# Kernel tuning notes

Hardware: AMD Instinct MI355X
Metric: run time of the kernel (lower is better)

## Reference

```python
import jax, jax.numpy as jnp
import numpy as np

B, SQ, SKV, D = 8, 2048, 2048, 1024

def setup_inputs() -> dict:
    key = jax.random.key(0)
    ks = jax.random.split(key, 8)
    s = 1.0 / np.sqrt(D)  # torch Linear default init range
    return {
        "target": jax.random.normal(ks[0], (B, SQ, D), dtype=jnp.float32),
        "non_target": jax.random.normal(ks[1], (B, SKV, D), dtype=jnp.float32),
        "Wq": jax.random.uniform(ks[2], (D, D), jnp.float32, -s, s),
        "bq": jax.random.uniform(ks[3], (D,), jnp.float32, -s, s),
        "Wk": jax.random.uniform(ks[4], (D, D), jnp.float32, -s, s),
        "bk": jax.random.uniform(ks[5], (D,), jnp.float32, -s, s),
        "Wv": jax.random.uniform(ks[6], (D, D), jnp.float32, -s, s),
        "bv": jax.random.uniform(ks[7], (D,), jnp.float32, -s, s),
    }

def reference(target, non_target, Wq, bq, Wk, bk, Wv, bv):
    # Linear projections (torch Linear: x @ W.T + b)
    q = jnp.einsum('bsd,ed->bse', target, Wq) + bq       # [B,SQ,D]
    k = jnp.einsum('bsd,ed->bse', non_target, Wk) + bk   # [B,SKV,D]
    v = jnp.einsum('bsd,ed->bse', non_target, Wv) + bv   # [B,SKV,D]
    # Unscaled attention, exactly as the original module (no 1/sqrt(d))
    scores = jnp.einsum('bqd,bkd->bqk', q, k)            # [B,SQ,SKV]
    weights = jax.nn.softmax(scores, axis=-1)
    return jnp.einsum('bqk,bkd->bqd', weights, v)        # [B,SQ,D]
```

## Files before the change

### kernel.cpp

```cpp
#include <hip/hip_runtime.h>


typedef _Float16 half8 __attribute__((ext_vector_type(8)));
typedef _Float16 half4v __attribute__((ext_vector_type(4)));
typedef float floatx4 __attribute__((ext_vector_type(4)));

__device__ __forceinline__ void async_copy16(const _Float16* g, _Float16* l) {
  __builtin_amdgcn_global_load_lds(
      (const __attribute__((address_space(1))) void*)g,
      (__attribute__((address_space(3))) void*)l,
      16, 0, 0);
}

__global__ __launch_bounds__(256) void cast_f32_f16(const float* __restrict__ src,
                                                    _Float16* __restrict__ dst, long n) {
  long i = ((long)blockIdx.x * 256 + threadIdx.x) * 8;
  if (i >= n) return;
  float4 a = *(const float4*)(src + i);
  float4 b = *(const float4*)(src + i + 4);
  half8 h;
  h[0] = (_Float16)a.x; h[1] = (_Float16)a.y; h[2] = (_Float16)a.z; h[3] = (_Float16)a.w;
  h[4] = (_Float16)b.x; h[5] = (_Float16)b.y; h[6] = (_Float16)b.z; h[7] = (_Float16)b.w;
  *(half8*)(dst + i) = h;
}


#define GSLICE(KC, AFC, BFC, AFN, BFN)                                          \
  {                                                                             \
    const int kc_ = (KC);                                                       \
    int ks_ = kc_ + 3; if (ks_ > NK - 1) ks_ = NK - 1;                          \
    int pf_ = kc_ + 1; if (pf_ > NK - 1) pf_ = NK - 1;                          \
    _Float16* sa_ = Ar + (ks_ & 3) * 8192 + ldst;                               \
    _Float16* sb_ = Br + (ks_ & 3) * 8192 + ldst;                               \
    const long go_ = (long)ks_ * 32;                                            \
    async_copy16(Abg + go_, sa_);                                               \
    async_copy16(Abg + go_ + lK128, sa_ + 4096);                                \
    async_copy16(Bbg + go_, sb_);                                               \
    async_copy16(Bbg + go_ + lK128, sb_ + 4096);                                \
    const _Float16* pa_ = Ar + (pf_ & 3) * 8192 + wm * 4096 + aoff;             \
    const _Float16* pb_ = Br + (pf_ & 3) * 8192 + wn * 2048 + aoff;             \
    _Pragma("unroll") for (int n = 0; n < 4; ++n)                               \
      BFN[n] = *(const half8*)(pb_ + n * 512);                                  \
    _Pragma("unroll") for (int i = 0; i < 8; ++i)                               \
      AFN[i] = *(const half8*)(pa_ + (i & 3) * 512 + (i >> 2) * 2048);          \
    __builtin_amdgcn_sched_barrier(0);                                          \
    __builtin_amdgcn_s_setprio(1);                                              \
    _Pragma("unroll") for (int i = 0; i < 8; ++i)                               \
      _Pragma("unroll") for (int n = 0; n < 4; ++n)                             \
        acc[i][n] = __builtin_amdgcn_mfma_f32_16x16x32_f16(AFC[i], BFC[n],      \
                                                           acc[i][n], 0, 0, 0); \
    __builtin_amdgcn_s_setprio(0);                                              \
    asm volatile("s_waitcnt lgkmcnt(0)" ::: "memory");                          \
    __builtin_amdgcn_sched_barrier(0);                                          \
    asm volatile("s_waitcnt vmcnt(4)" ::: "memory");                            \
    __builtin_amdgcn_s_barrier();                                               \
  }

template <int OMODE>
__global__ __launch_bounds__(512, 2) void gemm256(const _Float16* __restrict__ A,
                                                  const _Float16* __restrict__ Bm,
                                                  const float* __restrict__ bias,
                                                  void* __restrict__ out,
                                                  int K, int N,
                                                  long sA, long sB, long sO) {
  __shared__ __attribute__((aligned(16))) _Float16 lds[65536];
  _Float16* Ar = lds;
  _Float16* Br = lds + 32768;

  const int tid = threadIdx.x;
  const int lane = tid & 63;
  const int wave = tid >> 6;
  const int wm = wave >> 2;
  const int wn = wave & 3;
  const int frow = lane & 15;
  const int fq = (lane >> 4) & 3;
  const long bz = blockIdx.z;

  const int glog = (tid & 7) ^ ((tid >> 3) & 7);
  const long sg = (long)(2 * (tid >> 3) + (glog >> 2)) * K + (glog & 3) * 8;
  const int ldst = tid * 8;
  const long lK128 = (long)K * 128;

  const _Float16* Abg = A + bz * sA + (long)blockIdx.x * 256 * K + sg;
  const _Float16* Bbg = Bm + bz * sB + (long)blockIdx.y * 256 * K + sg;

  const int gphys = ((frow & 1) * 4 + fq) ^ (frow >> 1);
  const int aoff = (frow >> 1) * 64 + gphys * 8;

  floatx4 acc[8][4];
#pragma unroll
  for (int m = 0; m < 8; ++m)
#pragma unroll
    for (int n = 0; n < 4; ++n) acc[m][n] = (floatx4){0.f, 0.f, 0.f, 0.f};

  const int NK = K >> 5;

#pragma unroll
  for (int kp = 0; kp < 3; ++kp) {
    async_copy16(Abg + kp * 32, Ar + kp * 8192 + ldst);
    async_copy16(Abg + kp * 32 + lK128, Ar + kp * 8192 + ldst + 4096);
    async_copy16(Bbg + kp * 32, Br + kp * 8192 + ldst);
    async_copy16(Bbg + kp * 32 + lK128, Br + kp * 8192 + ldst + 4096);
  }
  asm volatile("s_waitcnt vmcnt(4)" ::: "memory");
  __builtin_amdgcn_s_barrier();

  half8 afA[8], bfA[4], afB[8], bfB[4];
  {
    const _Float16* pa = Ar + wm * 4096 + aoff;
    const _Float16* pb = Br + wn * 2048 + aoff;
#pragma unroll
    for (int n = 0; n < 4; ++n) bfA[n] = *(const half8*)(pb + n * 512);
#pragma unroll
    for (int i = 0; i < 8; ++i) afA[i] = *(const half8*)(pa + (i & 3) * 512 + (i >> 2) * 2048);
  }
  asm volatile("s_waitcnt lgkmcnt(0)" ::: "memory");
  __builtin_amdgcn_sched_barrier(0);

  for (int kc = 0; kc < NK; kc += 2) {
    GSLICE(kc, afA, bfA, afB, bfB);
    GSLICE(kc + 1, afB, bfB, afA, bfA);
  }

  if (OMODE == 0 || OMODE == 1) {
#pragma unroll
    for (int n = 0; n < 4; ++n) {
      const int cg = blockIdx.y * 256 + wn * 64 + n * 16 + frow;
      const float bvv = bias[cg];
#pragma unroll
      for (int m = 0; m < 8; ++m) {
        const int rg = blockIdx.x * 256 + wm * 128 + m * 16 + fq * 4;
        if (OMODE == 0) {
#pragma unroll
          for (int i = 0; i < 4; ++i)
            ((_Float16*)out)[(long)(rg + i) * N + cg] = (_Float16)(acc[m][n][i] + bvv);
        } else {
          const long bb = rg >> 11;
          const int s = rg & 2047;
          half4v hv;
#pragma unroll
          for (int i = 0; i < 4; ++i) hv[i] = (_Float16)(acc[m][n][i] + bvv);
          *(half4v*)((_Float16*)out + bb * (2048l * 1024) + (long)cg * 2048 + s) = hv;
        }
      }
    }
  } else {
#pragma unroll
    for (int n = 0; n < 4; ++n) {
      const int cg = blockIdx.y * 256 + wn * 64 + n * 16 + frow;
#pragma unroll
      for (int m = 0; m < 8; ++m) {
        const int rgl = blockIdx.x * 256 + wm * 128 + m * 16 + fq * 4;
#pragma unroll
        for (int i = 0; i < 4; ++i) {
          if (OMODE == 2)
            ((float*)out + bz * sO)[(long)(rgl + i) * N + cg] = acc[m][n][i];
          else
            ((_Float16*)out + bz * sO)[(long)(rgl + i) * N + cg] = (_Float16)acc[m][n][i];
        }
      }
    }
  }
}

__global__ __launch_bounds__(256) void softmax_rows(const _Float16* __restrict__ S,
                                                    _Float16* __restrict__ P) {
  const long row = blockIdx.x;
  const _Float16* src = S + row * 2048;
  _Float16* dst = P + row * 2048;
  const int tid = threadIdx.x;

  half8 v = ((const half8*)src)[tid];
  float f[8];
#pragma unroll
  for (int i = 0; i < 8; i++) f[i] = (float)v[i];

  float m = fmaxf(fmaxf(fmaxf(f[0], f[1]), fmaxf(f[2], f[3])),
                  fmaxf(fmaxf(f[4], f[5]), fmaxf(f[6], f[7])));
#pragma unroll
  for (int o = 32; o > 0; o >>= 1) m = fmaxf(m, __shfl_xor(m, o, 64));
  __shared__ float redm[4];
  if ((tid & 63) == 0) redm[tid >> 6] = m;
  __syncthreads();
  m = fmaxf(fmaxf(redm[0], redm[1]), fmaxf(redm[2], redm[3]));

  float e[8], s = 0.f;
#pragma unroll
  for (int i = 0; i < 8; i++) { e[i] = __expf(f[i] - m); s += e[i]; }
#pragma unroll
  for (int o = 32; o > 0; o >>= 1) s += __shfl_xor(s, o, 64);
  __shared__ float reds[4];
  if ((tid & 63) == 0) reds[tid >> 6] = s;
  __syncthreads();
  s = (reds[0] + reds[1]) + (reds[2] + reds[3]);
  const float inv = 1.f / s;

  half8 h;
#pragma unroll
  for (int i = 0; i < 8; i++) h[i] = (_Float16)(e[i] * inv);
  ((half8*)dst)[tid] = h;
}

extern "C" void kernel_launch(void* const* d_in, const int* in_sizes, int n_in,
                              void* d_out, int out_size, void* d_ws, size_t ws_size,
                              hipStream_t stream) {
  const float* target = (const float*)d_in[0];
  const float* non_target = (const float*)d_in[1];
  const float* Wq = (const float*)d_in[2];
  const float* bq = (const float*)d_in[3];
  const float* Wk = (const float*)d_in[4];
  const float* bk = (const float*)d_in[5];
  const float* Wv = (const float*)d_in[6];
  const float* bv = (const float*)d_in[7];

  char* ws = (char*)d_ws;
  const size_t MB = 1ull << 20;
  _Float16* tgt16 = (_Float16*)(ws);
  _Float16* ntg16 = (_Float16*)(ws + 32 * MB);
  _Float16* S16 = (_Float16*)(ws);
  _Float16* P16 = (_Float16*)(ws + 64 * MB);
  _Float16* Q16 = (_Float16*)(ws + 128 * MB);
  _Float16* K16 = (_Float16*)(ws + 160 * MB);
  _Float16* Vt16 = (_Float16*)(ws + 192 * MB);
  _Float16* Wq16 = (_Float16*)(ws + 224 * MB);
  _Float16* Wk16 = (_Float16*)(ws + 226 * MB);
  _Float16* Wv16 = (_Float16*)(ws + 228 * MB);

  const long nBig = 8l * 2048 * 1024;
  const long nW = 1024l * 1024;

  cast_f32_f16<<<8192, 256, 0, stream>>>(target, tgt16, nBig);
  cast_f32_f16<<<8192, 256, 0, stream>>>(non_target, ntg16, nBig);
  cast_f32_f16<<<512, 256, 0, stream>>>(Wq, Wq16, nW);
  cast_f32_f16<<<512, 256, 0, stream>>>(Wk, Wk16, nW);
  cast_f32_f16<<<512, 256, 0, stream>>>(Wv, Wv16, nW);

  gemm256<0><<<dim3(64, 4, 1), 512, 0, stream>>>(tgt16, Wq16, bq, Q16, 1024, 1024, 0, 0, 0);
  gemm256<0><<<dim3(64, 4, 1), 512, 0, stream>>>(ntg16, Wk16, bk, K16, 1024, 1024, 0, 0, 0);
  gemm256<1><<<dim3(64, 4, 1), 512, 0, stream>>>(ntg16, Wv16, bv, Vt16, 1024, 1024, 0, 0, 0);

  gemm256<3><<<dim3(8, 8, 8), 512, 0, stream>>>(Q16, K16, nullptr, S16, 1024, 2048,
                                                2048l * 1024, 2048l * 1024, 2048l * 2048);

  softmax_rows<<<16384, 256, 0, stream>>>(S16, P16);

  gemm256<2><<<dim3(8, 4, 8), 512, 0, stream>>>(P16, Vt16, nullptr, (float*)d_out, 2048, 1024,
                                                2048l * 2048, 1024l * 2048, 2048l * 1024);
}
```

Baseline: 488.3 us.

## Fuse input casts and softmax normalization into GEMM A-tile loads

The fp32-to-fp16 casts of target and non_target move into the projection GEMMs: the A tile is loaded as fp32 into registers, converted, and written to LDS instead of using async global-to-LDS copies. The softmax kernel now writes only per-row max and inverse sum, and the P·V GEMM applies exp and scaling while staging S into LDS, so the P buffer is never written or read. Block index swizzling is added to the score and output GEMMs to improve L2 reuse. The cost is register-path loads and extra ALU work inside the GEMM main loop, which may weaken the async pipeline's overlap. The exp is also recomputed once per column block of the output GEMM.

```diff
diff --git a/kernel.cpp b/kernel.cpp
--- a/kernel.cpp
+++ b/kernel.cpp
@@ -33,10 +33,21 @@
     _Float16* sa_ = Ar + (ks_ & 3) * 8192 + ldst;                               \
     _Float16* sb_ = Br + (ks_ & 3) * 8192 + ldst;                               \
     const long go_ = (long)ks_ * 32;                                            \
-    async_copy16(Abg + go_, sa_);                                               \
-    async_copy16(Abg + go_ + lK128, sa_ + 4096);                                \
-    async_copy16(Bbg + go_, sb_);                                               \
-    async_copy16(Bbg + go_ + lK128, sb_ + 4096);                                \
+    floatx4 qa0_, qa1_, qb0_, qb1_; half8 ha_, hb_;                             \
+    if (ATRANS == 0) {                                                          \
+      async_copy16(Ah + go_, sa_);                                              \
+      async_copy16(Ah + go_ + lK128, sa_ + 4096);                               \
+    } else if (ATRANS == 1) {                                                   \
+      qa0_ = *(const floatx4*)(Af + go_);                                       \
+      qa1_ = *(const floatx4*)(Af + go_ + 4);                                   \
+      qb0_ = *(const floatx4*)(Af + go_ + lK128);                               \
+      qb1_ = *(const floatx4*)(Af + go_ + lK128 + 4);                           \
+    } else {                                                                    \
+      ha_ = *(const half8*)(Ah + go_);                                          \
+      hb_ = *(const half8*)(Ah + go_ + lK128);                                  \
+    }                                                                           \
+    async_copy16(Bh + go_, sb_);                                                \
+    async_copy16(Bh + go_ + lK128, sb_ + 4096);                                 \
     const _Float16* pa_ = Ar + (pf_ & 3) * 8192 + wm * 4096 + aoff;             \
     const _Float16* pb_ = Br + (pf_ & 3) * 8192 + wn * 2048 + aoff;             \
     _Pragma("unroll") for (int n = 0; n < 4; ++n)                               \
@@ -50,16 +61,33 @@
         acc[i][n] = __builtin_amdgcn_mfma_f32_16x16x32_f16(AFC[i], BFC[n],      \
                                                            acc[i][n], 0, 0, 0); \
     __builtin_amdgcn_s_setprio(0);                                              \
+    __builtin_amdgcn_sched_barrier(0);                                          \
+    if (ATRANS == 1) {                                                          \
+      half8 w0_, w1_;                                                           \
+      _Pragma("unroll") for (int t = 0; t < 4; ++t) {                           \
+        w0_[t] = (_Float16)qa0_[t]; w0_[4 + t] = (_Float16)qa1_[t];             \
+        w1_[t] = (_Float16)qb0_[t]; w1_[4 + t] = (_Float16)qb1_[t]; }           \
+      *(half8*)sa_ = w0_; *(half8*)(sa_ + 4096) = w1_;                          \
+    } else if (ATRANS == 2) {                                                   \
+      half8 w0_, w1_;                                                           \
+      _Pragma("unroll") for (int t = 0; t < 8; ++t) {                           \
+        w0_[t] = (_Float16)(__expf((float)ha_[t] - mA0) * sA0);                 \
+        w1_[t] = (_Float16)(__expf((float)hb_[t] - mA1) * sA1); }               \
+      *(half8*)sa_ = w0_; *(half8*)(sa_ + 4096) = w1_;                          \
+    }                                                                           \
     asm volatile("s_waitcnt lgkmcnt(0)" ::: "memory");                          \
     __builtin_amdgcn_sched_barrier(0);                                          \
-    asm volatile("s_waitcnt vmcnt(4)" ::: "memory");                            \
+    if (ATRANS == 0) { asm volatile("s_waitcnt vmcnt(4)" ::: "memory"); }       \
+    else             { asm volatile("s_waitcnt vmcnt(2)" ::: "memory"); }       \
     __builtin_amdgcn_s_barrier();                                               \
   }
 
-template <int OMODE>
-__global__ __launch_bounds__(512, 2) void gemm256(const _Float16* __restrict__ A,
+template <int OMODE, int ATRANS, int SWZ>
+__global__ __launch_bounds__(512, 2) void gemm256(const void* __restrict__ A,
                                                   const _Float16* __restrict__ Bm,
                                                   const float* __restrict__ bias,
+                                                  const float* __restrict__ rowM,
+                                                  const float* __restrict__ rowS,
                                                   void* __restrict__ out,
                                                   int K, int N,
                                                   long sA, long sB, long sO) {
@@ -76,13 +104,35 @@
   const int fq = (lane >> 4) & 3;
   const long bz = blockIdx.z;
 
+  int bx = blockIdx.x, by = blockIdx.y;
+  if (SWZ == 1) {
+    int h = bx + 8 * by, g = h & 7, idx = h >> 3;
+    bx = (g & 3) * 2 + (idx & 1);
+    by = (g >> 2) * 4 + (idx >> 1);
+  } else if (SWZ == 2) {
+    int h = bx + 8 * by, g = h & 7, idx = h >> 3;
+    bx = (g & 3) * 2 + (idx & 1);
+    by = (g >> 2) * 2 + (idx >> 1);
+  }
+
   const int glog = (tid & 7) ^ ((tid >> 3) & 7);
   const long sg = (long)(2 * (tid >> 3) + (glog >> 2)) * K + (glog & 3) * 8;
   const int ldst = tid * 8;
   const long lK128 = (long)K * 128;
 
-  const _Float16* Abg = A + bz * sA + (long)blockIdx.x * 256 * K + sg;
-  const _Float16* Bbg = Bm + bz * sB + (long)blockIdx.y * 256 * K + sg;
+  const _Float16* Ah = (ATRANS != 1) ? (const _Float16*)A + bz * sA + (long)bx * 256 * K + sg
+                                     : nullptr;
+  const float* Af = (ATRANS == 1) ? (const float*)A + bz * sA + (long)bx * 256 * K + sg
+                                  : nullptr;
+  const _Float16* Bh = Bm + bz * sB + (long)by * 256 * K + sg;
+
+  float mA0 = 0.f, sA0 = 0.f, mA1 = 0.f, sA1 = 0.f;
+  if (ATRANS == 2) {
+    const int rA0 = 2 * (tid >> 3) + (glog >> 2);
+    const long gr = bz * 2048 + (long)bx * 256 + rA0;
+    mA0 = rowM[gr]; sA0 = rowS[gr];
+    mA1 = rowM[gr + 128]; sA1 = rowS[gr + 128];
+  }
 
   const int gphys = ((frow & 1) * 4 + fq) ^ (frow >> 1);
   const int aoff = (frow >> 1) * 64 + gphys * 8;
@@ -97,11 +147,37 @@
 
 #pragma unroll
   for (int kp = 0; kp < 3; ++kp) {
-    async_copy16(Abg + kp * 32, Ar + kp * 8192 + ldst);
-    async_copy16(Abg + kp * 32 + lK128, Ar + kp * 8192 + ldst + 4096);
-    async_copy16(Bbg + kp * 32, Br + kp * 8192 + ldst);
-    async_copy16(Bbg + kp * 32 + lK128, Br + kp * 8192 + ldst + 4096);
-  }
+    _Float16* sa = Ar + kp * 8192 + ldst;
+    if (ATRANS == 0) {
+      async_copy16(Ah + kp * 32, sa);
+      async_copy16(Ah + kp * 32 + lK128, sa + 4096);
+    } else if (ATRANS == 1) {
+      floatx4 a0 = *(const floatx4*)(Af + kp * 32);
+      floatx4 a1 = *(const floatx4*)(Af + kp * 32 + 4);
+      floatx4 b0 = *(const floatx4*)(Af + kp * 32 + lK128);
+      floatx4 b1 = *(const floatx4*)(Af + kp * 32 + lK128 + 4);
+      half8 w0, w1;
+#pragma unroll
+      for (int t = 0; t < 4; ++t) {
+        w0[t] = (_Float16)a0[t]; w0[4 + t] = (_Float16)a1[t];
+        w1[t] = (_Float16)b0[t]; w1[4 + t] = (_Float16)b1[t];
+      }
+      *(half8*)sa = w0; *(half8*)(sa + 4096) = w1;
+    } else {
+      half8 h0 = *(const half8*)(Ah + kp * 32);
+      half8 h1 = *(const half8*)(Ah + kp * 32 + lK128);
+      half8 w0, w1;
+#pragma unroll
+      for (int t = 0; t < 8; ++t) {
+        w0[t] = (_Float16)(__expf((float)h0[t] - mA0) * sA0);
+        w1[t] = (_Float16)(__expf((float)h1[t] - mA1) * sA1);
+      }
+      *(half8*)sa = w0; *(half8*)(sa + 4096) = w1;
+    }
+    async_copy16(Bh + kp * 32, Br + kp * 8192 + ldst);
+    async_copy16(Bh + kp * 32 + lK128, Br + kp * 8192 + ldst + 4096);
+  }
+  asm volatile("s_waitcnt lgkmcnt(0)" ::: "memory");
   asm volatile("s_waitcnt vmcnt(4)" ::: "memory");
   __builtin_amdgcn_s_barrier();
 
@@ -125,11 +201,11 @@
   if (OMODE == 0 || OMODE == 1) {
 #pragma unroll
     for (int n = 0; n < 4; ++n) {
-      const int cg = blockIdx.y * 256 + wn * 64 + n * 16 + frow;
+      const int cg = by * 256 + wn * 64 + n * 16 + frow;
       const float bvv = bias[cg];
 #pragma unroll
       for (int m = 0; m < 8; ++m) {
-        const int rg = blockIdx.x * 256 + wm * 128 + m * 16 + fq * 4;
+        const int rg = bx * 256 + wm * 128 + m * 16 + fq * 4;
         if (OMODE == 0) {
 #pragma unroll
           for (int i = 0; i < 4; ++i)
@@ -147,10 +223,10 @@
   } else {
 #pragma unroll
     for (int n = 0; n < 4; ++n) {
-      const int cg = blockIdx.y * 256 + wn * 64 + n * 16 + frow;
+      const int cg = by * 256 + wn * 64 + n * 16 + frow;
 #pragma unroll
       for (int m = 0; m < 8; ++m) {
-        const int rgl = blockIdx.x * 256 + wm * 128 + m * 16 + fq * 4;
+        const int rgl = bx * 256 + wm * 128 + m * 16 + fq * 4;
 #pragma unroll
         for (int i = 0; i < 4; ++i) {
           if (OMODE == 2)
@@ -163,11 +239,11 @@
   }
 }
 
-__global__ __launch_bounds__(256) void softmax_rows(const _Float16* __restrict__ S,
-                                                    _Float16* __restrict__ P) {
+__global__ __launch_bounds__(256) void rowstat(const _Float16* __restrict__ S,
+                                               float* __restrict__ rowM,
+                                               float* __restrict__ rowS) {
   const long row = blockIdx.x;
   const _Float16* src = S + row * 2048;
-  _Float16* dst = P + row * 2048;
   const int tid = threadIdx.x;
 
   half8 v = ((const half8*)src)[tid];
@@ -184,21 +260,20 @@
   __syncthreads();
   m = fmaxf(fmaxf(redm[0], redm[1]), fmaxf(redm[2], redm[3]));
 
-  float e[8], s = 0.f;
-#pragma unroll
-  for (int i = 0; i < 8; i++) { e[i] = __expf(f[i] - m); s += e[i]; }
+  float s = 0.f;
+#pragma unroll
+  for (int i = 0; i < 8; i++) s += __expf(f[i] - m);
 #pragma unroll
   for (int o = 32; o > 0; o >>= 1) s += __shfl_xor(s, o, 64);
   __shared__ float reds[4];
   if ((tid & 63) == 0) reds[tid >> 6] = s;
   __syncthreads();
   s = (reds[0] + reds[1]) + (reds[2] + reds[3]);
-  const float inv = 1.f / s;
-
-  half8 h;
-#pragma unroll
-  for (int i = 0; i < 8; i++) h[i] = (_Float16)(e[i] * inv);
-  ((half8*)dst)[tid] = h;
+
+  if (tid == 0) {
+    rowM[row] = m;
+    rowS[row] = 1.f / s;
+  }
 }
 
 extern "C" void kernel_launch(void* const* d_in, const int* in_sizes, int n_in,
@@ -215,10 +290,9 @@
 
   char* ws = (char*)d_ws;
   const size_t MB = 1ull << 20;
-  _Float16* tgt16 = (_Float16*)(ws);
-  _Float16* ntg16 = (_Float16*)(ws + 32 * MB);
   _Float16* S16 = (_Float16*)(ws);
-  _Float16* P16 = (_Float16*)(ws + 64 * MB);
+  float* mrow = (float*)(ws + 64 * MB);
+  float* srow = (float*)(ws + 65 * MB);
   _Float16* Q16 = (_Float16*)(ws + 128 * MB);
   _Float16* K16 = (_Float16*)(ws + 160 * MB);
   _Float16* Vt16 = (_Float16*)(ws + 192 * MB);
@@ -226,24 +300,26 @@
   _Float16* Wk16 = (_Float16*)(ws + 226 * MB);
   _Float16* Wv16 = (_Float16*)(ws + 228 * MB);
 
-  const long nBig = 8l * 2048 * 1024;
   const long nW = 1024l * 1024;
 
-  cast_f32_f16<<<8192, 256, 0, stream>>>(target, tgt16, nBig);
-  cast_f32_f16<<<8192, 256, 0, stream>>>(non_target, ntg16, nBig);
   cast_f32_f16<<<512, 256, 0, stream>>>(Wq, Wq16, nW);
   cast_f32_f16<<<512, 256, 0, stream>>>(Wk, Wk16, nW);
   cast_f32_f16<<<512, 256, 0, stream>>>(Wv, Wv16, nW);
 
-  gemm256<0><<<dim3(64, 4, 1), 512, 0, stream>>>(tgt16, Wq16, bq, Q16, 1024, 1024, 0, 0, 0);
-  gemm256<0><<<dim3(64, 4, 1), 512, 0, stream>>>(ntg16, Wk16, bk, K16, 1024, 1024, 0, 0, 0);
-  gemm256<1><<<dim3(64, 4, 1), 512, 0, stream>>>(ntg16, Wv16, bv, Vt16, 1024, 1024, 0, 0, 0);
-
-  gemm256<3><<<dim3(8, 8, 8), 512, 0, stream>>>(Q16, K16, nullptr, S16, 1024, 2048,
-                                                2048l * 1024, 2048l * 1024, 2048l * 2048);
-
-  softmax_rows<<<16384, 256, 0, stream>>>(S16, P16);
-
-  gemm256<2><<<dim3(8, 4, 8), 512, 0, stream>>>(P16, Vt16, nullptr, (float*)d_out, 2048, 1024,
-                                                2048l * 2048, 1024l * 2048, 2048l * 1024);
-}
+  gemm256<0, 1, 0><<<dim3(64, 4, 1), 512, 0, stream>>>(target, Wq16, bq, nullptr, nullptr,
+                                                       Q16, 1024, 1024, 0, 0, 0);
+  gemm256<0, 1, 0><<<dim3(64, 4, 1), 512, 0, stream>>>(non_target, Wk16, bk, nullptr, nullptr,
+                                                       K16, 1024, 1024, 0, 0, 0);
+  gemm256<1, 1, 0><<<dim3(64, 4, 1), 512, 0, stream>>>(non_target, Wv16, bv, nullptr, nullptr,
+                                                       Vt16, 1024, 1024, 0, 0, 0);
+
+  gemm256<3, 0, 1><<<dim3(8, 8, 8), 512, 0, stream>>>(Q16, K16, nullptr, nullptr, nullptr,
+                                                      S16, 1024, 2048,
+                                                      2048l * 1024, 2048l * 1024, 2048l * 2048);
+
+  rowstat<<<16384, 256, 0, stream>>>(S16, mrow, srow);
+
+  gemm256<2, 2, 2><<<dim3(8, 4, 8), 512, 0, stream>>>(S16, Vt16, nullptr, mrow, srow,
+                                                      (float*)d_out, 2048, 1024,
+                                                      2048l * 2048, 1024l * 2048, 2048l * 1024);
+}
```

New measurement: 508.0 us. +4.0%, slower.
